# Kernel optimization log

Measured on AMD Instinct MI355X. Metric: run time of the kernel, lower is better.

The kernel has to match this reference:

```python
import jax, jax.numpy as jnp
import numpy as np

N_HEADS = 12


def setup_inputs() -> dict:
    key = jax.random.key(0)
    ks = jax.random.split(key, 5)
    B, T, D = 4, 2048, 768
    std = 1.0 / np.sqrt(D)
    return {
        "x": jax.random.normal(ks[0], (B, T, D), jnp.float32),
        "W_qkv": jax.random.normal(ks[1], (3 * D, D), jnp.float32) * std,
        "b_qkv": jax.random.normal(ks[2], (3 * D,), jnp.float32) * 0.02,
        "W_proj": jax.random.normal(ks[3], (D, D), jnp.float32) * std,
        "b_proj": jax.random.normal(ks[4], (D,), jnp.float32) * 0.02,
    }


def reference(x, W_qkv, b_qkv, W_proj, b_proj):
    # x: [B, T, D]; intended 3D path of the module (dropout = eval-mode identity)
    B, T, D = x.shape
    H = N_HEADS
    Dh = D // H
    scale = Dh ** -0.5
    qkv = x @ W_qkv.T + b_qkv                       # [B, T, 3D]
    qkv = qkv.reshape(B, T, 3, H, Dh)
    q = jnp.transpose(qkv[:, :, 0], (0, 2, 1, 3))    # [B, H, T, Dh]
    k = jnp.transpose(qkv[:, :, 1], (0, 2, 1, 3))
    v = jnp.transpose(qkv[:, :, 2], (0, 2, 1, 3))
    attn = jnp.einsum("bhqd,bhkd->bhqk", q, k) * scale  # [B, H, T, T]
    scores = jax.nn.softmax(attn, axis=-1)
    out = jnp.einsum("bhqk,bhkd->bhqd", scores, v)       # [B, H, T, Dh]
    out = jnp.transpose(out, (0, 2, 1, 3)).reshape(B, T, D)
    return out @ W_proj.T + b_proj
```

## Files before the change

### kernel.cpp

```cpp
#include <hip/hip_runtime.h>
#include <hip/hip_bf16.h>
#include <stdint.h>

typedef __bf16 bf16;
typedef __bf16 bf16x8 __attribute__((ext_vector_type(8)));
typedef __bf16 bf16x4 __attribute__((ext_vector_type(4)));
typedef short  s16x4  __attribute__((ext_vector_type(4)));
typedef short  s16x8  __attribute__((ext_vector_type(8)));
typedef float  f32x4  __attribute__((ext_vector_type(4)));

#define N_B 4
#define N_T 2048
#define N_D 768
#define N_H 12
#define N_DH 64
#define M_TOT (N_B * N_T)

__device__ __forceinline__ void async_copy16(const bf16* g, bf16* l) {
    __builtin_amdgcn_global_load_lds(
        (const __attribute__((address_space(1))) unsigned int*)g,
        (__attribute__((address_space(3))) unsigned int*)l,
        16, 0, 0);
}

__launch_bounds__(256)
__global__ void f2bf3(const float* __restrict__ a, bf16* __restrict__ oa, int na,
                      const float* __restrict__ b, bf16* __restrict__ ob, int nb,
                      const float* __restrict__ c, bf16* __restrict__ oc) {
    int i = (blockIdx.x * 256 + threadIdx.x) * 4;
    const float* src; bf16* dst;
    if (i < na)            { src = a; dst = oa; }
    else if (i < na + nb)  { src = b; dst = ob; i -= na; }
    else                   { src = c; dst = oc; i -= na + nb; }
    const float4 v = *(const float4*)(src + i);
    dst[i]     = (bf16)v.x;
    dst[i + 1] = (bf16)v.y;
    dst[i + 2] = (bf16)v.z;
    dst[i + 3] = (bf16)v.w;
}

#define GEMM_CORE(A_PTR, B_PTR, KDIM)                                          \
    __shared__ bf16 lsA[128 * 32];                                             \
    __shared__ bf16 lsB[128 * 32];                                             \
    const int m0 = blockIdx.x * 128;                                           \
    const int n0 = blockIdx.y * 128;                                           \
    const int t  = threadIdx.x;                                                \
    const int w  = t >> 6, l = t & 63;                                         \
    const int wm = w & 1, wn = w >> 1;                                         \
    const int lr = l & 15, lq = l >> 4;                                        \
    f32x4 acc[4][4] = {};                                                      \
    const bf16* Ab = (A_PTR) + (size_t)(m0 + (t >> 2)) * (KDIM) + (t & 3) * 8; \
    const bf16* Bb = (B_PTR) + (size_t)(n0 + (t >> 2)) * (KDIM) + (t & 3) * 8; \
    bf16* lA = lsA + t * 8;                                                    \
    bf16* lB = lsB + t * 8;                                                    \
    for (int k0 = 0; k0 < (KDIM); k0 += 32) {                                  \
        __syncthreads();                                                       \
        async_copy16(Ab + k0, lA);                                             \
        async_copy16(Ab + (size_t)64 * (KDIM) + k0, lA + 2048);                \
        async_copy16(Bb + k0, lB);                                             \
        async_copy16(Bb + (size_t)64 * (KDIM) + k0, lB + 2048);                \
        __syncthreads();                                                       \
        bf16x8 af[4], bfr[4];                                                  \
        for (int i = 0; i < 4; i++) {                                          \
            af[i]  = *(const bf16x8*)(lsA + (wm * 64 + i * 16 + lr) * 32 + lq * 8); \
            bfr[i] = *(const bf16x8*)(lsB + (wn * 64 + i * 16 + lr) * 32 + lq * 8); \
        }                                                                      \
        for (int i = 0; i < 4; i++)                                            \
            for (int j = 0; j < 4; j++)                                        \
                acc[i][j] = __builtin_amdgcn_mfma_f32_16x16x32_bf16(           \
                    af[i], bfr[j], acc[i][j], 0, 0, 0);                        \
    }

__launch_bounds__(256)
__global__ void gemm_qkv(const bf16* __restrict__ X, const bf16* __restrict__ W,
                         const float* __restrict__ bias,
                         bf16* __restrict__ Q, bf16* __restrict__ K,
                         bf16* __restrict__ Vt) {
    GEMM_CORE(X, W, 768)
    for (int i = 0; i < 4; i++) {
        const int rowb = m0 + wm * 64 + i * 16 + lq * 4;
        const int b_ = rowb >> 11, tt = rowb & 2047;
        for (int j = 0; j < 4; j++) {
            const int col   = n0 + wn * 64 + j * 16 + lr;
            const int which = col / 768;
            const int rem   = col - which * 768;
            const int h     = rem >> 6, d = rem & 63;
            const float bv  = bias[col];
            if (which == 2) {
                const int tile = tt >> 6, kl = tt & 63;
                const int kc = kl >> 4, r = kl & 15;
                const int idx = ((r >> 2) << 4) + (kc << 2);
                bf16x4 v4;
                for (int r2 = 0; r2 < 4; r2++) v4[r2] = (bf16)(acc[i][j][r2] + bv);
                *(bf16x4*)(Vt + ((size_t)((b_ * N_H + h) * 64 + d)) * 2048
                           + tile * 64 + idx) = v4;
            } else {
                bf16* dst = (which == 0) ? Q : K;
                const float sc = (which == 0) ? 0.18033688f : 1.0f;
                for (int r2 = 0; r2 < 4; r2++)
                    dst[(size_t)(((b_ * N_H + h) << 11) + tt + r2) * 64 + d] =
                        (bf16)((acc[i][j][r2] + bv) * sc);
            }
        }
    }
}

__launch_bounds__(256)
__global__ void gemm_proj(const bf16* __restrict__ O, const bf16* __restrict__ W,
                          const float* __restrict__ bias, float* __restrict__ out) {
    GEMM_CORE(O, W, 768)
    for (int i = 0; i < 4; i++) {
        const int rowb = m0 + wm * 64 + i * 16 + lq * 4;
        for (int j = 0; j < 4; j++) {
            const int col  = n0 + wn * 64 + j * 16 + lr;
            const float bv = bias[col];
            for (int r = 0; r < 4; r++)
                out[(size_t)(rowb + r) * 768 + col] = acc[i][j][r] + bv;
        }
    }
}

__launch_bounds__(512, 6)
__global__ void attn(const bf16* __restrict__ Q, const bf16* __restrict__ K,
                     const bf16* __restrict__ Vt, bf16* __restrict__ O) {
    __shared__ bf16 lsK[2][64 * 64];
    __shared__ bf16 lsV[3][64 * 64];
    const int bid = blockIdx.x;
    const int xcd = bid & 7, slot = bid >> 3;
    const int bh  = xcd + 8 * (slot >> 4);
    const int qt  = slot & 15;
    const int t = threadIdx.x, w = t >> 6, l = t & 63;
    const int lr = l & 15, lq = l >> 4;
    const bf16* Qh  = Q  + (size_t)bh * N_T * 64;
    const bf16* Kh  = K  + (size_t)bh * N_T * 64;
    const bf16* Vth = Vt + (size_t)bh * 64 * N_T;
    const int q0 = qt * 128 + w * 16;

    const int sr = t >> 3;
    const int sp = t & 7;
    const int scn = sp ^ (sr & 7);

    bf16x8 qf[2];
    for (int ks = 0; ks < 2; ks++)
        qf[ks] = *(const bf16x8*)(Qh + (size_t)(q0 + lr) * 64 + ks * 32 + lq * 8);

    f32x4 oacc[4] = {};
    f32x4 lacc = {};
    const s16x4 ones = {0x3F80, 0x3F80, 0x3F80, 0x3F80};

    async_copy16(Kh  + (size_t)sr * 64 + scn * 8,   lsK[0] + t * 8);
    async_copy16(Vth + (size_t)sr * 2048 + scn * 8, lsV[0] + t * 8);
    __syncthreads();
    async_copy16(Kh  + (size_t)(64 + sr) * 64 + scn * 8, lsK[1] + t * 8);
    async_copy16(Vth + (size_t)sr * 2048 + 64 + scn * 8, lsV[1] + t * 8);

    f32x4 sprev[4] = {};
    for (int ks = 0; ks < 2; ks++)
        for (int ki = 0; ki < 4; ki++) {
            bf16x8 kf = *(const bf16x8*)(lsK[0] + (ki * 16 + lr) * 64
                                         + ((ks * 4 + lq) ^ (lr & 7)) * 8);
            sprev[ki] = __builtin_amdgcn_mfma_f32_16x16x32_bf16(
                kf, qf[ks], sprev[ki], 0, 0, 0);
        }

    int vprev = 0, vcur = 1, vnext = 2;

    for (int i = 1; i < 32; i++) {
        __syncthreads();

        if (i < 31) {
            async_copy16(Kh  + (size_t)((i + 1) * 64 + sr) * 64 + scn * 8,
                         lsK[(i + 1) & 1] + t * 8);
            async_copy16(Vth + (size_t)sr * 2048 + (i + 1) * 64 + scn * 8,
                         lsV[vnext] + t * 8);
        }

        f32x4 snew[4] = {};
        for (int ks = 0; ks < 2; ks++)
            for (int ki = 0; ki < 4; ki++) {
                bf16x8 kf = *(const bf16x8*)(lsK[i & 1] + (ki * 16 + lr) * 64
                                             + ((ks * 4 + lq) ^ (lr & 7)) * 8);
                snew[ki] = __builtin_amdgcn_mfma_f32_16x16x32_bf16(
                    kf, qf[ks], snew[ki], 0, 0, 0);
            }

        s16x4 pbf[4];
        for (int ki = 0; ki < 4; ki++) {
            bf16x4 pb;
            for (int r = 0; r < 4; r++)
                pb[r] = (bf16)exp2f(sprev[ki][r]);
            pbf[ki] = __builtin_bit_cast(s16x4, pb);
        }

        const bf16* vb = lsV[vprev];
        for (int c = 0; c < 2; c++)
            for (int dj = 0; dj < 4; dj++) {
                const int unit = (2 * lq + c) ^ (lr & 7);
                s16x8 vv = *(const s16x8*)(vb + (dj * 16 + lr) * 64 + unit * 8);
                s16x4 vlo = __builtin_shufflevector(vv, vv, 0, 1, 2, 3);
                s16x4 vhi = __builtin_shufflevector(vv, vv, 4, 5, 6, 7);
                oacc[dj] = __builtin_amdgcn_mfma_f32_16x16x16bf16_1k(
                    vlo, pbf[2 * c], oacc[dj], 0, 0, 0);
                oacc[dj] = __builtin_amdgcn_mfma_f32_16x16x16bf16_1k(
                    vhi, pbf[2 * c + 1], oacc[dj], 0, 0, 0);
            }
        for (int kc = 0; kc < 4; kc++)
            lacc = __builtin_amdgcn_mfma_f32_16x16x16bf16_1k(
                ones, pbf[kc], lacc, 0, 0, 0);

        for (int ki = 0; ki < 4; ki++) sprev[ki] = snew[ki];
        const int tmp = vprev; vprev = vcur; vcur = vnext; vnext = tmp;
    }

    {
        s16x4 pbf[4];
        for (int ki = 0; ki < 4; ki++) {
            bf16x4 pb;
            for (int r = 0; r < 4; r++)
                pb[r] = (bf16)exp2f(sprev[ki][r]);
            pbf[ki] = __builtin_bit_cast(s16x4, pb);
        }
        const bf16* vb = lsV[vprev];
        for (int c = 0; c < 2; c++)
            for (int dj = 0; dj < 4; dj++) {
                const int unit = (2 * lq + c) ^ (lr & 7);
                s16x8 vv = *(const s16x8*)(vb + (dj * 16 + lr) * 64 + unit * 8);
                s16x4 vlo = __builtin_shufflevector(vv, vv, 0, 1, 2, 3);
                s16x4 vhi = __builtin_shufflevector(vv, vv, 4, 5, 6, 7);
                oacc[dj] = __builtin_amdgcn_mfma_f32_16x16x16bf16_1k(
                    vlo, pbf[2 * c], oacc[dj], 0, 0, 0);
                oacc[dj] = __builtin_amdgcn_mfma_f32_16x16x16bf16_1k(
                    vhi, pbf[2 * c + 1], oacc[dj], 0, 0, 0);
            }
        for (int kc = 0; kc < 4; kc++)
            lacc = __builtin_amdgcn_mfma_f32_16x16x16bf16_1k(
                ones, pbf[kc], lacc, 0, 0, 0);
    }

    const int b = bh / N_H, h = bh - b * N_H;
    const float inv_l = 1.0f / lacc[0];
    const int tok = q0 + lr;
    bf16* Ob = O + ((size_t)b * N_T + tok) * N_D + h * 64;
    for (int dj = 0; dj < 4; dj++) {
        bf16x4 o4;
        for (int r = 0; r < 4; r++) o4[r] = (bf16)(oacc[dj][r] * inv_l);
        *(bf16x4*)(Ob + dj * 16 + lq * 4) = o4;
    }
}

extern "C" void kernel_launch(void* const* d_in, const int* in_sizes, int n_in,
                              void* d_out, int out_size, void* d_ws, size_t ws_size,
                              hipStream_t stream) {
    const float* x      = (const float*)d_in[0];
    const float* W_qkv  = (const float*)d_in[1];
    const float* b_qkv  = (const float*)d_in[2];
    const float* W_proj = (const float*)d_in[3];
    const float* b_proj = (const float*)d_in[4];
    float* out = (float*)d_out;

    char* ws = (char*)d_ws;
    const size_t n_x  = (size_t)M_TOT * N_D;
    const size_t n_wq = (size_t)3 * N_D * N_D;
    const size_t n_wp = (size_t)N_D * N_D;
    const size_t sz_qkv = (size_t)N_B * N_H * N_T * N_DH * sizeof(bf16);

    bf16* xb  = (bf16*)(ws);                 ws += n_x * sizeof(bf16);
    bf16* Wqb = (bf16*)(ws);                 ws += n_wq * sizeof(bf16);
    bf16* Wpb = (bf16*)(ws);                 ws += n_wp * sizeof(bf16);
    bf16* Qb  = (bf16*)(ws);                 ws += sz_qkv;
    bf16* Kb  = (bf16*)(ws);                 ws += sz_qkv;
    bf16* Vtb = (bf16*)(ws);                 ws += sz_qkv;
    bf16* Ob  = (bf16*)(ws);

    dim3 blk(256);
    f2bf3<<<dim3((int)((n_x + n_wq + n_wp) / 1024)), blk, 0, stream>>>(
        x, xb, (int)n_x, W_qkv, Wqb, (int)n_wq, W_proj, Wpb);

    gemm_qkv<<<dim3(M_TOT / 128, 2304 / 128), blk, 0, stream>>>(xb, Wqb, b_qkv, Qb, Kb, Vtb);
    attn<<<dim3(768), dim3(512), 0, stream>>>(Qb, Kb, Vtb, Ob);
    gemm_proj<<<dim3(M_TOT / 128, 768 / 128), blk, 0, stream>>>(Ob, Wpb, b_proj, out);
}
```

Measured before the change: 234.5 us.

## Stage QKV epilogue through LDS for coalesced stores; read K directly from global

The QKV GEMM epilogue now branches once per block on Q/K versus V. For Q and K it stages the biased, scaled tile in shared memory with padded rows and writes it back as 16-byte vectors per token, replacing scattered 2-byte stores. The attention kernel drops the K shared-memory double buffer and loads K fragments straight from global memory, which frees LDS and cuts async copies but leaves K reads exposed to cache latency inside the loop. The GEMM shared allocation grows to hold the staging tile.

```diff
diff --git a/kernel.cpp b/kernel.cpp
--- a/kernel.cpp
+++ b/kernel.cpp
@@ -40,8 +40,9 @@
 }
 
 #define GEMM_CORE(A_PTR, B_PTR, KDIM)                                          \
-    __shared__ bf16 lsA[128 * 32];                                             \
-    __shared__ bf16 lsB[128 * 32];                                             \
+    __shared__ bf16 smem[9216];                                                \
+    bf16* lsA = smem;                                                          \
+    bf16* lsB = smem + 4096;                                                   \
     const int m0 = blockIdx.x * 128;                                           \
     const int n0 = blockIdx.y * 128;                                           \
     const int t  = threadIdx.x;                                                \
@@ -77,29 +78,49 @@
                          bf16* __restrict__ Q, bf16* __restrict__ K,
                          bf16* __restrict__ Vt) {
     GEMM_CORE(X, W, 768)
-    for (int i = 0; i < 4; i++) {
-        const int rowb = m0 + wm * 64 + i * 16 + lq * 4;
-        const int b_ = rowb >> 11, tt = rowb & 2047;
-        for (int j = 0; j < 4; j++) {
-            const int col   = n0 + wn * 64 + j * 16 + lr;
-            const int which = col / 768;
-            const int rem   = col - which * 768;
-            const int h     = rem >> 6, d = rem & 63;
-            const float bv  = bias[col];
-            if (which == 2) {
-                const int tile = tt >> 6, kl = tt & 63;
-                const int kc = kl >> 4, r = kl & 15;
-                const int idx = ((r >> 2) << 4) + (kc << 2);
+    const int which = n0 / 768;
+    const int b_ = m0 >> 11, tt0 = m0 & 2047;
+    if (which == 2) {
+        for (int i = 0; i < 4; i++) {
+            const int tt = tt0 + wm * 64 + i * 16 + lq * 4;
+            const int tile = tt >> 6, kl = tt & 63;
+            const int kc = kl >> 4, r = kl & 15;
+            const int idx = ((r >> 2) << 4) + (kc << 2);
+            for (int j = 0; j < 4; j++) {
+                const int rem = n0 - 1536 + wn * 64 + j * 16 + lr;
+                const int h = rem >> 6, d = rem & 63;
+                const float bv = bias[n0 + wn * 64 + j * 16 + lr];
                 bf16x4 v4;
                 for (int r2 = 0; r2 < 4; r2++) v4[r2] = (bf16)(acc[i][j][r2] + bv);
                 *(bf16x4*)(Vt + ((size_t)((b_ * N_H + h) * 64 + d)) * 2048
                            + tile * 64 + idx) = v4;
-            } else {
-                bf16* dst = (which == 0) ? Q : K;
-                const float sc = (which == 0) ? 0.18033688f : 1.0f;
-                for (int r2 = 0; r2 < 4; r2++)
-                    dst[(size_t)(((b_ * N_H + h) << 11) + tt + r2) * 64 + d] =
-                        (bf16)((acc[i][j][r2] + bv) * sc);
+            }
+        }
+    } else {
+        bf16* dst0 = (which == 0) ? Q : K;
+        const float sc = (which == 0) ? 0.18033688f : 1.0f;
+        const int rem0 = n0 - which * 768;
+        for (int p = 0; p < 2; p++) {
+            __syncthreads();
+            if (wn == p) {
+                for (int i = 0; i < 4; i++)
+                    for (int j = 0; j < 4; j++) {
+                        const int cL = j * 16 + lr;
+                        const float bv = bias[n0 + p * 64 + cL];
+                        const int tokL = wm * 64 + i * 16 + lq * 4;
+                        for (int r = 0; r < 4; r++)
+                            smem[(tokL + r) * 72 + cL] =
+                                (bf16)((acc[i][j][r] + bv) * sc);
+                    }
+            }
+            __syncthreads();
+            {
+                const int token = t >> 1, dh = (t & 1) * 32;
+                const int h = (rem0 >> 6) + p;
+                bf16* dp = dst0 + ((size_t)(((b_ * N_H + h) << 11) + tt0 + token)) * 64 + dh;
+                const bf16* sp2 = smem + token * 72 + dh;
+                for (int c = 0; c < 4; c++)
+                    *(bf16x8*)(dp + c * 8) = *(const bf16x8*)(sp2 + c * 8);
             }
         }
     }
@@ -123,7 +144,6 @@
 __launch_bounds__(512, 6)
 __global__ void attn(const bf16* __restrict__ Q, const bf16* __restrict__ K,
                      const bf16* __restrict__ Vt, bf16* __restrict__ O) {
-    __shared__ bf16 lsK[2][64 * 64];
     __shared__ bf16 lsV[3][64 * 64];
     const int bid = blockIdx.x;
     const int xcd = bid & 7, slot = bid >> 3;
@@ -140,6 +160,8 @@
     const int sp = t & 7;
     const int scn = sp ^ (sr & 7);
 
+    const bf16* Kb = Kh + (size_t)lr * 64 + lq * 8;
+
     bf16x8 qf[2];
     for (int ks = 0; ks < 2; ks++)
         qf[ks] = *(const bf16x8*)(Qh + (size_t)(q0 + lr) * 64 + ks * 32 + lq * 8);
@@ -148,17 +170,14 @@
     f32x4 lacc = {};
     const s16x4 ones = {0x3F80, 0x3F80, 0x3F80, 0x3F80};
 
-    async_copy16(Kh  + (size_t)sr * 64 + scn * 8,   lsK[0] + t * 8);
     async_copy16(Vth + (size_t)sr * 2048 + scn * 8, lsV[0] + t * 8);
     __syncthreads();
-    async_copy16(Kh  + (size_t)(64 + sr) * 64 + scn * 8, lsK[1] + t * 8);
     async_copy16(Vth + (size_t)sr * 2048 + 64 + scn * 8, lsV[1] + t * 8);
 
     f32x4 sprev[4] = {};
     for (int ks = 0; ks < 2; ks++)
         for (int ki = 0; ki < 4; ki++) {
-            bf16x8 kf = *(const bf16x8*)(lsK[0] + (ki * 16 + lr) * 64
-                                         + ((ks * 4 + lq) ^ (lr & 7)) * 8);
+            bf16x8 kf = *(const bf16x8*)(Kb + ki * 1024 + ks * 32);
             sprev[ki] = __builtin_amdgcn_mfma_f32_16x16x32_bf16(
                 kf, qf[ks], sprev[ki], 0, 0, 0);
         }
@@ -168,18 +187,14 @@
     for (int i = 1; i < 32; i++) {
         __syncthreads();
 
-        if (i < 31) {
-            async_copy16(Kh  + (size_t)((i + 1) * 64 + sr) * 64 + scn * 8,
-                         lsK[(i + 1) & 1] + t * 8);
+        if (i < 31)
             async_copy16(Vth + (size_t)sr * 2048 + (i + 1) * 64 + scn * 8,
                          lsV[vnext] + t * 8);
-        }
 
         f32x4 snew[4] = {};
         for (int ks = 0; ks < 2; ks++)
             for (int ki = 0; ki < 4; ki++) {
-                bf16x8 kf = *(const bf16x8*)(lsK[i & 1] + (ki * 16 + lr) * 64
-                                             + ((ks * 4 + lq) ^ (lr & 7)) * 8);
+                bf16x8 kf = *(const bf16x8*)(Kb + (size_t)i * 4096 + ki * 1024 + ks * 32);
                 snew[ki] = __builtin_amdgcn_mfma_f32_16x16x32_bf16(
                     kf, qf[ks], snew[ki], 0, 0, 0);
             }
```

Measured after the change: 330.9 us. +41.1%, slower.
